# Kernel optimization log

Measured on AMD Instinct MI355X. Metric: run time of the kernel, lower is better.

## Reference

```python
import jax, jax.numpy as jnp
import numpy as np

DIM = 1024
HEADS = 16
DIM_HEAD = 64
INNER = HEADS * DIM_HEAD  # 1024
MLP = 4096
EPS = 1e-5


def setup_inputs() -> dict:
    key = jax.random.key(0)
    ks = jax.random.split(key, 8)
    s = lambda fan_in: 1.0 / np.sqrt(fan_in)
    return {
        "x": jax.random.normal(ks[0], (4, 2048, DIM), dtype=jnp.float32),
        "ln1_g": jnp.ones((DIM,), jnp.float32),
        "ln1_b": jnp.zeros((DIM,), jnp.float32),
        "w_qkv": jax.random.normal(ks[1], (DIM, 3 * INNER), jnp.float32) * s(DIM),
        "w_out": jax.random.normal(ks[2], (INNER, DIM), jnp.float32) * s(INNER),
        "b_out": jnp.zeros((DIM,), jnp.float32),
        "ln2_g": jnp.ones((DIM,), jnp.float32),
        "ln2_b": jnp.zeros((DIM,), jnp.float32),
        "w1": jax.random.normal(ks[3], (DIM, MLP), jnp.float32) * s(DIM),
        "b1": jnp.zeros((MLP,), jnp.float32),
        "w2": jax.random.normal(ks[4], (MLP, DIM), jnp.float32) * s(MLP),
        "b2": jnp.zeros((DIM,), jnp.float32),
    }


def _layernorm(x, g, b):
    mu = jnp.mean(x, axis=-1, keepdims=True)
    var = jnp.mean(jnp.square(x - mu), axis=-1, keepdims=True)
    return (x - mu) * jax.lax.rsqrt(var + EPS) * g + b


def _block(x, ln1_g, ln1_b, w_qkv, w_out, b_out, ln2_g, ln2_b, w1, b1, w2, b2):
    # pre-norm attention
    h = _layernorm(x, ln1_g, ln1_b)
    qkv = h @ w_qkv  # [b, n, 3*inner]
    q, k, v = jnp.split(qkv, 3, axis=-1)
    def heads(t):  # b n (h d) -> b h n d
        b, n, _ = t.shape
        return t.reshape(b, n, HEADS, DIM_HEAD).transpose(0, 2, 1, 3)
    q, k, v = heads(q), heads(k), heads(v)
    scale = DIM_HEAD ** -0.5
    dots = jnp.einsum("bhnd,bhmd->bhnm", q, k) * scale
    attn = jax.nn.softmax(dots, axis=-1)
    out = jnp.einsum("bhnm,bhmd->bhnd", attn, v)
    b, _, n, _ = out.shape
    out = out.transpose(0, 2, 1, 3).reshape(b, n, INNER)
    x = out @ w_out + b_out + x
    # pre-norm FFN
    h = _layernorm(x, ln2_g, ln2_b)
    h = jax.nn.gelu(h @ w1 + b1, approximate=False)
    return h @ w2 + b2 + x


def reference(x, ln1_g, ln1_b, w_qkv, w_out, b_out, ln2_g, ln2_b, w1, b1, w2, b2):
    return _block(x, ln1_g, ln1_b, w_qkv, w_out, b_out, ln2_g, ln2_b, w1, b1, w2, b2)
```

## Files before the change

### kernel.cpp

```cpp
#include <hip/hip_runtime.h>
#include <hip/hip_bf16.h>
#include <math.h>


typedef __bf16 bf16;
typedef __bf16 bf16x8 __attribute__((ext_vector_type(8)));
typedef __bf16 bf16x4 __attribute__((ext_vector_type(4)));
typedef __bf16 bf16x2 __attribute__((ext_vector_type(2)));
typedef float  f32x4  __attribute__((ext_vector_type(4)));
typedef unsigned int u32;
typedef u32 u32x4 __attribute__((ext_vector_type(4)));

#define MFMA_16x16x32(a, b, c) __builtin_amdgcn_mfma_f32_16x16x32_bf16((a), (b), (c), 0, 0, 0)

#define SWAP32(x, y) asm("v_permlane32_swap_b32 %0, %1" : "+v"(x), "+v"(y))
#define SWAP16(x, y) asm("v_permlane16_swap_b32 %0, %1" : "+v"(x), "+v"(y))

__device__ __forceinline__ void gl_lds16(const void* g, void* l) {
    __builtin_amdgcn_global_load_lds(
        (const __attribute__((address_space(1))) u32*)g,
        (__attribute__((address_space(3))) u32*)l, 16, 0, 0);
}

__device__ __forceinline__ u32 pack_bf16x2(float a, float b) {
    bf16x2 t; t[0] = (bf16)a; t[1] = (bf16)b;
    return __builtin_bit_cast(u32, t);
}

__device__ __forceinline__ float fast_gelu(float x) {
    const float u = x * (0.7978845608028654f + 0.03567740814183f * x * x);
    const float e = __builtin_amdgcn_exp2f(u * 2.8853900817779268f);
    return x * e * __builtin_amdgcn_rcpf(e + 1.0f);
}

__global__ __launch_bounds__(256) void transpose_f32_bf16(
    const float* __restrict__ in, bf16* __restrict__ out, int R, int C)
{
    __shared__ float tile[32][33];
    const int cb = blockIdx.x * 32, rb = blockIdx.y * 32;
    const int c = threadIdx.x & 31, r0 = threadIdx.x >> 5;
#pragma unroll
    for (int i = 0; i < 4; ++i) {
        int r = r0 + i * 8;
        tile[r][c] = in[(size_t)(rb + r) * C + cb + c];
    }
    __syncthreads();
#pragma unroll
    for (int i = 0; i < 4; ++i) {
        int rr = r0 + i * 8;
        out[(size_t)(cb + rr) * R + rb + c] = (bf16)tile[c][rr];
    }
}

__global__ __launch_bounds__(256) void transpose_v(
    const bf16* __restrict__ qkv, bf16* __restrict__ VT)
{
    __shared__ float tile[32][33];
    const int tokb = blockIdx.x * 32;
    const int db   = blockIdx.y * 32;
    const int bh   = blockIdx.z;
    const int b = bh >> 4, h = bh & 15;
    const int c = threadIdx.x & 31, r0 = threadIdx.x >> 5;
#pragma unroll
    for (int i = 0; i < 4; ++i) {
        int r = r0 + i * 8;
        tile[r][c] = (float)qkv[(size_t)(b * 2048 + tokb + r) * 3072 + 2048 + h * 64 + db + c];
    }
    __syncthreads();
#pragma unroll
    for (int i = 0; i < 4; ++i) {
        int rr = r0 + i * 8;
        VT[((size_t)bh * 64 + db + rr) * 2048 + tokb + c] = (bf16)tile[c][rr];
    }
}

__global__ __launch_bounds__(256) void ln_kernel(
    const float* __restrict__ x, const float* __restrict__ g,
    const float* __restrict__ b, bf16* __restrict__ out)
{
    const int lane = threadIdx.x & 63;
    const int wv   = threadIdx.x >> 6;
    const size_t token = (size_t)blockIdx.x * 4 + wv;
    const float* xr = x + token * 1024;
    float4 v[4];
    float s = 0.f, ss = 0.f;
#pragma unroll
    for (int c = 0; c < 4; ++c) {
        v[c] = *(const float4*)(xr + c * 256 + lane * 4);
        s  += v[c].x + v[c].y + v[c].z + v[c].w;
        ss += v[c].x * v[c].x + v[c].y * v[c].y + v[c].z * v[c].z + v[c].w * v[c].w;
    }
#pragma unroll
    for (int off = 32; off > 0; off >>= 1) {
        s  += __shfl_xor(s, off);
        ss += __shfl_xor(ss, off);
    }
    const float mu  = s * (1.0f / 1024.0f);
    const float var = ss * (1.0f / 1024.0f) - mu * mu;
    const float rs  = rsqrtf(var + 1e-5f);
    bf16* orow = out + token * 1024;
#pragma unroll
    for (int c = 0; c < 4; ++c) {
        float4 gg = *(const float4*)(g + c * 256 + lane * 4);
        float4 bb = *(const float4*)(b + c * 256 + lane * 4);
        bf16x4 o;
        o[0] = (bf16)((v[c].x - mu) * rs * gg.x + bb.x);
        o[1] = (bf16)((v[c].y - mu) * rs * gg.y + bb.y);
        o[2] = (bf16)((v[c].z - mu) * rs * gg.z + bb.z);
        o[3] = (bf16)((v[c].w - mu) * rs * gg.w + bb.w);
        *(bf16x4*)(orow + c * 256 + lane * 4) = o;
    }
}

template <int EPI>
__global__ __launch_bounds__(256, 4) void gemm_bt(
    const bf16* __restrict__ A, const bf16* __restrict__ Bt,
    const float* __restrict__ bias, const float* __restrict__ resid,
    void* __restrict__ outp, int M, int N, int K)
{
    __shared__ __align__(16) bf16 sA[128 * 64];
    __shared__ __align__(16) bf16 sB[128 * 64];

    const int tid  = threadIdx.x;
    const int lane = tid & 63;
    const int wv   = tid >> 6;
    const int quad = lane >> 4;
    const int l16  = lane & 15;

    const int id  = blockIdx.x;
    const int xcd = id & 7, j = id >> 3;
    const int M0 = (xcd * 8 + (j & 7)) * 128;
    const int N0 = (j >> 3) * 128;

    const int wm = (wv >> 1) * 64;
    const int wn = (wv & 1) * 64;

    f32x4 acc[4][4] = {};

    const bf16* paG[4];
    const bf16* pbG[4];
#pragma unroll
    for (int c = 0; c < 4; ++c) {
        const int f = c * 256 + tid;
        const int row = f >> 3;
        const int gch = (f & 7) ^ (row & 7);
        paG[c] = A  + (size_t)(M0 + row) * K + gch * 8;
        pbG[c] = Bt + (size_t)(N0 + row) * K + gch * 8;
    }

    const int sw = l16 & 7;

    for (int k0 = 0; k0 < K; k0 += 64) {
        __syncthreads();
#pragma unroll
        for (int c = 0; c < 4; ++c) {
            const int f8 = (c * 256 + tid) * 8;
            gl_lds16(paG[c] + k0, sA + f8);
            gl_lds16(pbG[c] + k0, sB + f8);
        }
        __syncthreads();

#pragma unroll
        for (int s = 0; s < 2; ++s) {
            const int chp = (s * 4 + quad) ^ sw;
            bf16x8 af[4], bfr[4];
#pragma unroll
            for (int t = 0; t < 4; ++t)
                af[t] = *(const bf16x8*)(sA + ((wm + t * 16 + l16) << 6) + chp * 8);
#pragma unroll
            for (int t = 0; t < 4; ++t)
                bfr[t] = *(const bf16x8*)(sB + ((wn + t * 16 + l16) << 6) + chp * 8);
#pragma unroll
            for (int tm = 0; tm < 4; ++tm)
#pragma unroll
                for (int tn = 0; tn < 4; ++tn)
                    acc[tm][tn] = MFMA_16x16x32(bfr[tn], af[tm], acc[tm][tn]);
        }
    }

#pragma unroll
    for (int tm = 0; tm < 4; ++tm) {
        const int row = M0 + wm + tm * 16 + l16;
#pragma unroll
        for (int tn = 0; tn < 4; ++tn) {
            const int col = N0 + wn + tn * 16 + quad * 4;
            const size_t idx = (size_t)row * N + col;
            const f32x4 v = acc[tm][tn];
            if (EPI == 0) {
                bf16x4 o;
#pragma unroll
                for (int r = 0; r < 4; ++r) o[r] = (bf16)v[r];
                *(bf16x4*)((bf16*)outp + idx) = o;
            } else if (EPI == 1) {
                const f32x4 b4 = *(const f32x4*)(bias + col);
                const f32x4 r4 = *(const f32x4*)(resid + idx);
                *(f32x4*)((float*)outp + idx) = v + b4 + r4;
            } else {
                const f32x4 b4 = *(const f32x4*)(bias + col);
                bf16x4 o;
#pragma unroll
                for (int r = 0; r < 4; ++r) o[r] = (bf16)fast_gelu(v[r] + b4[r]);
                *(bf16x4*)((bf16*)outp + idx) = o;
            }
        }
    }
}

#define BAR256()  asm volatile("s_barrier" ::: "memory")
#define WAITVM(n) asm volatile("s_waitcnt vmcnt(" #n ")" ::: "memory")
#define WAITLG()  do { asm volatile("s_waitcnt lgkmcnt(0)" ::: "memory"); \
                       __builtin_amdgcn_sched_barrier(0); } while (0)

template <int EPI>
__global__ __launch_bounds__(512, 2) void gemm256(
    const bf16* __restrict__ A, const bf16* __restrict__ Bt,
    const float* __restrict__ bias, void* __restrict__ outp,
    int N, int K)
{
    __shared__ __align__(16) bf16 sA[2][16384];
    __shared__ __align__(16) bf16 sB[2][16384];

    const int tid  = threadIdx.x;
    const int lane = tid & 63;
    const int wv   = tid >> 6;
    const int quad = lane >> 4;
    const int l16  = lane & 15;
    const int wr   = wv >> 2;
    const int wc   = wv & 3;

    const int id = blockIdx.x;
    const int wg = (id & 7) * ((int)gridDim.x >> 3) + (id >> 3);
    const int M0 = (wg & 31) * 256;
    const int N0 = (wg >> 5) * 256;

    const int srow = tid >> 3;
    const int sch  = (tid & 7) ^ (srow & 7);
    const bf16* gA = A  + (size_t)(M0 + srow) * K + sch * 8;
    const bf16* gB = Bt + (size_t)(N0 + srow) * K + sch * 8;
    const size_t r64  = (size_t)64 * K;
    const size_t r128 = (size_t)128 * K;

    f32x4 acc[8][4] = {};
    bf16x8 af[4][2], bf0[2][2], bf1[2][2];

    auto STG = [&](const bf16* g, bf16* l) {
        gl_lds16(g, l + tid * 8);
        gl_lds16(g + r64, l + tid * 8 + 4096);
    };
    auto LDA = [&](int buf, int mh) {
#pragma unroll
        for (int tm = 0; tm < 4; ++tm) {
            const int row = wr * 128 + mh * 64 + tm * 16 + l16;
            const bf16* p = &sA[buf][row * 64];
            const int swz = (row & 7) << 3;
            af[tm][0] = *(const bf16x8*)(p + (( quad      << 3) ^ swz));
            af[tm][1] = *(const bf16x8*)(p + (((quad + 4) << 3) ^ swz));
        }
    };
    auto LDB = [&](int buf, int nh, bf16x8 (&bfr)[2][2]) {
#pragma unroll
        for (int tn = 0; tn < 2; ++tn) {
            const int row = wc * 64 + nh * 32 + tn * 16 + l16;
            const bf16* p = &sB[buf][row * 64];
            const int swz = (row & 7) << 3;
            bfr[tn][0] = *(const bf16x8*)(p + (( quad      << 3) ^ swz));
            bfr[tn][1] = *(const bf16x8*)(p + (((quad + 4) << 3) ^ swz));
        }
    };
    auto MM = [&](int mh, int nh, bf16x8 (&bfr)[2][2]) {
        __builtin_amdgcn_s_setprio(1);
#pragma unroll
        for (int tm = 0; tm < 4; ++tm)
#pragma unroll
            for (int tn = 0; tn < 2; ++tn) {
                f32x4& a = acc[mh * 4 + tm][nh * 2 + tn];
                a = MFMA_16x16x32(bfr[tn][0], af[tm][0], a);
                a = MFMA_16x16x32(bfr[tn][1], af[tm][1], a);
            }
        __builtin_amdgcn_s_setprio(0);
    };

    STG(gA,              &sA[0][0]);
    STG(gA + r128,       &sA[0][8192]);
    STG(gB,              &sB[0][0]);
    STG(gB + r128,       &sB[0][8192]);
    STG(gB + 64,         &sB[1][0]);
    STG(gB + r128 + 64,  &sB[1][8192]);
    WAITVM(4);
    BAR256();

    const int NU = K >> 7;
#pragma unroll 1
    for (int u = 0; u < NU; ++u) {
        const size_t k1 = (size_t)(2 * u + 1) * 64;
        const size_t k2 = (size_t)(2 * u + 2) * 64;
        const size_t k3 = (size_t)(2 * u + 3) * 64;
        const bool more = (u + 1 < NU);

        LDA(0, 0); LDB(0, 0, bf0);
        STG(gA + k1, &sA[1][0]);
        BAR256(); WAITLG(); MM(0, 0, bf0); BAR256();

        LDB(0, 1, bf1);
        STG(gA + r128 + k1, &sA[1][8192]);
        BAR256(); WAITLG(); MM(0, 1, bf1); BAR256();

        LDA(0, 1);
        if (more) STG(gB + k2, &sB[0][0]);
        BAR256(); WAITLG(); MM(1, 1, bf1); BAR256();

        if (more) STG(gB + r128 + k2, &sB[0][8192]);
        BAR256(); MM(1, 0, bf0);
        if (more) { WAITVM(4); } else { WAITVM(0); }
        BAR256();

        LDA(1, 0); LDB(1, 0, bf0);
        if (more) STG(gA + k2, &sA[0][0]);
        BAR256(); WAITLG(); MM(0, 0, bf0); BAR256();

        LDB(1, 1, bf1);
        if (more) STG(gA + r128 + k2, &sA[0][8192]);
        BAR256(); WAITLG(); MM(0, 1, bf1); BAR256();

        LDA(1, 1);
        if (more) STG(gB + k3, &sB[1][0]);
        BAR256(); WAITLG(); MM(1, 1, bf1); BAR256();

        if (more) {
            STG(gB + r128 + k3, &sB[1][8192]);
            BAR256(); MM(1, 0, bf0);
            WAITVM(4);
            BAR256();
        } else {
            BAR256(); MM(1, 0, bf0);
        }
    }

#pragma unroll
    for (int tm = 0; tm < 8; ++tm) {
        const int row = M0 + wr * 128 + (tm >> 2) * 64 + (tm & 3) * 16 + l16;
#pragma unroll
        for (int tn = 0; tn < 4; ++tn) {
            const int col = N0 + wc * 64 + (tn >> 1) * 32 + (tn & 1) * 16 + quad * 4;
            const size_t idx = (size_t)row * N + col;
            const f32x4 v = acc[tm][tn];
            if (EPI == 0) {
                bf16x4 o;
#pragma unroll
                for (int r = 0; r < 4; ++r) o[r] = (bf16)v[r];
                *(bf16x4*)((bf16*)outp + idx) = o;
            } else {
                const f32x4 b4 = *(const f32x4*)(bias + col);
                bf16x4 o;
#pragma unroll
                for (int r = 0; r < 4; ++r) o[r] = (bf16)fast_gelu(v[r] + b4[r]);
                *(bf16x4*)((bf16*)outp + idx) = o;
            }
        }
    }
}

__global__ __launch_bounds__(256, 4) void attn_kernel(
    const bf16* __restrict__ qkv, const bf16* __restrict__ VT,
    bf16* __restrict__ attn_out)
{
    __shared__ __align__(16) bf16 sK[4096];
    __shared__ __align__(16) bf16 sV[4096];

    const int bh = blockIdx.y, b = bh >> 4, h = bh & 15;
    const int tid = threadIdx.x, lane = tid & 63, wv = tid >> 6;
    const int quad = lane >> 4, l16 = lane & 15;
    const size_t tok0 = (size_t)b * 2048;
    const int q0 = blockIdx.x * 128 + wv * 32;

    bf16x8 qf[2][2];
#pragma unroll
    for (int mi = 0; mi < 2; ++mi)
#pragma unroll
        for (int c = 0; c < 2; ++c) {
            bf16x8 t = *(const bf16x8*)(qkv + (tok0 + q0 + mi * 16 + l16) * 3072 + h * 64 + c * 32 + quad * 8);
#pragma unroll
            for (int j = 0; j < 8; ++j) t[j] = (bf16)((float)t[j] * 0.18033688011112042f);
            qf[mi][c] = t;
        }

    f32x4 o[2][4] = {};
    float lsum[2] = {0.f, 0.f};

    const int fA = tid, fB = tid + 256;
    const int cKA = fA >> 8, keyA = (fA >> 2) & 63, qcA = fA & 3;
    const int cKB = fB >> 8, keyB = (fB >> 2) & 63, qcB = fB & 3;
    const int dVA = fA >> 3, ccA = fA & 7;
    const int dVB = fB >> 3, ccB = fB & 7;
    const bf16* Kb = qkv + 1024 + h * 64;
    const bf16* Vb = VT + (size_t)bh * 64 * 2048;

    for (int kt = 0; kt < 32; ++kt) {
        const int kb = kt * 64;
        __syncthreads();
        gl_lds16(Kb + (tok0 + kb + keyA) * 3072 + cKA * 32 + ((qcA ^ (keyA & 3)) * 8), sK + fA * 8);
        gl_lds16(Kb + (tok0 + kb + keyB) * 3072 + cKB * 32 + ((qcB ^ (keyB & 3)) * 8), sK + fB * 8);
        gl_lds16(Vb + (size_t)dVA * 2048 + kb + ((ccA ^ (dVA & 7)) * 8), sV + fA * 8);
        gl_lds16(Vb + (size_t)dVB * 2048 + kb + ((ccB ^ (dVB & 7)) * 8), sV + fB * 8);
        __syncthreads();

        u32 w[2][4][2];
        __builtin_amdgcn_s_setprio(1);
#pragma unroll
        for (int ct = 0; ct < 4; ++ct) {
            const int key = ct * 16 + l16;
            const int ch = quad ^ (l16 & 3);
            bf16x8 k0 = *(const bf16x8*)(sK + (key * 4 + ch) * 8);
            bf16x8 k1 = *(const bf16x8*)(sK + (256 + key * 4 + ch) * 8);
#pragma unroll
            for (int mi = 0; mi < 2; ++mi) {
                f32x4 z = {};
                z = MFMA_16x16x32(k0, qf[mi][0], z);
                z = MFMA_16x16x32(k1, qf[mi][1], z);
                float p0 = __builtin_amdgcn_exp2f(z[0]);
                float p1 = __builtin_amdgcn_exp2f(z[1]);
                float p2 = __builtin_amdgcn_exp2f(z[2]);
                float p3 = __builtin_amdgcn_exp2f(z[3]);
                lsum[mi] += (p0 + p1) + (p2 + p3);
                w[mi][ct][0] = pack_bf16x2(p0, p1);
                w[mi][ct][1] = pack_bf16x2(p2, p3);
            }
        }
        __builtin_amdgcn_s_setprio(0);

        bf16x8 pa[2][2];
#pragma unroll
        for (int mi = 0; mi < 2; ++mi) {
            u32 pw0[4], pw1[4];
#pragma unroll
            for (int c2 = 0; c2 < 2; ++c2) {
                u32 x = w[mi][0][c2], y = w[mi][1][c2];
                SWAP32(x, y); SWAP16(x, y);
                pw0[c2] = x; pw0[2 + c2] = y;
                u32 x2 = w[mi][2][c2], y2 = w[mi][3][c2];
                SWAP32(x2, y2); SWAP16(x2, y2);
                pw1[c2] = x2; pw1[2 + c2] = y2;
            }
            u32x4 t0 = {pw0[0], pw0[1], pw0[2], pw0[3]};
            u32x4 t1 = {pw1[0], pw1[1], pw1[2], pw1[3]};
            pa[mi][0] = __builtin_bit_cast(bf16x8, t0);
            pa[mi][1] = __builtin_bit_cast(bf16x8, t1);
        }

        __builtin_amdgcn_s_setprio(1);
#pragma unroll
        for (int dt = 0; dt < 4; ++dt) {
            const int d = dt * 16 + l16;
            bf16x8 v0 = *(const bf16x8*)(sV + (d * 8 + (quad ^ (l16 & 7))) * 8);
            bf16x8 v1 = *(const bf16x8*)(sV + (d * 8 + ((quad + 4) ^ (l16 & 7))) * 8);
#pragma unroll
            for (int mi = 0; mi < 2; ++mi) {
                o[mi][dt] = MFMA_16x16x32(pa[mi][0], v0, o[mi][dt]);
                o[mi][dt] = MFMA_16x16x32(pa[mi][1], v1, o[mi][dt]);
            }
        }
        __builtin_amdgcn_s_setprio(0);
    }

#pragma unroll
    for (int mi = 0; mi < 2; ++mi) {
        float t = lsum[mi];
        t += __shfl_xor(t, 16);
        t += __shfl_xor(t, 32);
        float rl[4];
#pragma unroll
        for (int r = 0; r < 4; ++r) rl[r] = 1.0f / __shfl(t, quad * 4 + r);
#pragma unroll
        for (int dt = 0; dt < 4; ++dt)
#pragma unroll
            for (int r = 0; r < 4; ++r) {
                const size_t tok = tok0 + q0 + mi * 16 + quad * 4 + r;
                attn_out[tok * 1024 + h * 64 + dt * 16 + l16] = (bf16)(o[mi][dt][r] * rl[r]);
            }
    }
}

extern "C" void kernel_launch(void* const* d_in, const int* in_sizes, int n_in,
                              void* d_out, int out_size, void* d_ws, size_t ws_size,
                              hipStream_t stream)
{
    const float* x     = (const float*)d_in[0];
    const float* ln1_g = (const float*)d_in[1];
    const float* ln1_b = (const float*)d_in[2];
    const float* w_qkv = (const float*)d_in[3];
    const float* w_out = (const float*)d_in[4];
    const float* b_out = (const float*)d_in[5];
    const float* ln2_g = (const float*)d_in[6];
    const float* ln2_b = (const float*)d_in[7];
    const float* w1    = (const float*)d_in[8];
    const float* b1    = (const float*)d_in[9];
    const float* w2    = (const float*)d_in[10];
    const float* b2    = (const float*)d_in[11];
    float* out = (float*)d_out;

    char* ws = (char*)d_ws;
    bf16*  h      = (bf16*)(ws);
    bf16*  big    = (bf16*)(ws + 16777216);
    bf16*  attn_o = (bf16*)(ws + 83886080);
    float* x_mid  = (float*)(ws + 100663296);
    bf16*  VT     = (bf16*)(ws + 100663296);
    bf16*  wT_qkv = (bf16*)(ws + 134217728);
    bf16*  wT_out = (bf16*)(ws + 140509184);
    bf16*  wT_1   = (bf16*)(ws + 142606336);
    bf16*  wT_2   = (bf16*)(ws + 150994944);

    transpose_f32_bf16<<<dim3(3072/32, 1024/32), 256, 0, stream>>>(w_qkv, wT_qkv, 1024, 3072);
    transpose_f32_bf16<<<dim3(1024/32, 1024/32), 256, 0, stream>>>(w_out, wT_out, 1024, 1024);
    transpose_f32_bf16<<<dim3(4096/32, 1024/32), 256, 0, stream>>>(w1,    wT_1,   1024, 4096);
    transpose_f32_bf16<<<dim3(1024/32, 4096/32), 256, 0, stream>>>(w2,    wT_2,   4096, 1024);

    ln_kernel<<<2048, 256, 0, stream>>>(x, ln1_g, ln1_b, h);

    gemm_bt<0><<<64 * 24, 256, 0, stream>>>(h, wT_qkv, nullptr, nullptr, big, 8192, 3072, 1024);

    transpose_v<<<dim3(64, 2, 64), 256, 0, stream>>>(big, VT);

    attn_kernel<<<dim3(16, 64), 256, 0, stream>>>(big, VT, attn_o);

    gemm_bt<1><<<64 * 8, 256, 0, stream>>>(attn_o, wT_out, b_out, x, x_mid, 8192, 1024, 1024);

    ln_kernel<<<2048, 256, 0, stream>>>(x_mid, ln2_g, ln2_b, h);

    gemm256<2><<<512, 512, 0, stream>>>(h, wT_1, b1, big, 4096, 1024);

    gemm_bt<1><<<64 * 8, 256, 0, stream>>>(big, wT_2, b2, x_mid, out, 8192, 1024, 4096);
}
```

Before: 505.8 us.

## Fuse weight transposes with first layernorm and rebalance FFN GEMM tile choices

The four weight-transpose launches and the first layernorm are merged into a single prep kernel that dispatches on block index, removing several launches. The W1 GEMM moves from the 256x256 kernel to the generic 128-tile gemm_bt with the GELU epilogue. The W2 GEMM (K=4096) now uses a new 256x128-tile variant of the 256-thread-pair kernel with a residual epilogue, so larger tiles serve the long-K reduction. This trades tile shapes between the two FFN GEMMs. With N=1024 the W2 grid is only 256 blocks, which risks underfilling the device.

```diff
diff --git a/kernel.cpp b/kernel.cpp
--- a/kernel.cpp
+++ b/kernel.cpp
@@ -33,11 +33,11 @@
     return x * e * __builtin_amdgcn_rcpf(e + 1.0f);
 }
 
-__global__ __launch_bounds__(256) void transpose_f32_bf16(
-    const float* __restrict__ in, bf16* __restrict__ out, int R, int C)
-{
-    __shared__ float tile[32][33];
-    const int cb = blockIdx.x * 32, rb = blockIdx.y * 32;
+__device__ __forceinline__ void transpose_body(
+    const float* __restrict__ in, bf16* __restrict__ out, int R, int C,
+    int bx, int by, float (*tile)[33])
+{
+    const int cb = bx * 32, rb = by * 32;
     const int c = threadIdx.x & 31, r0 = threadIdx.x >> 5;
 #pragma unroll
     for (int i = 0; i < 4; ++i) {
@@ -52,35 +52,13 @@
     }
 }
 
-__global__ __launch_bounds__(256) void transpose_v(
-    const bf16* __restrict__ qkv, bf16* __restrict__ VT)
-{
-    __shared__ float tile[32][33];
-    const int tokb = blockIdx.x * 32;
-    const int db   = blockIdx.y * 32;
-    const int bh   = blockIdx.z;
-    const int b = bh >> 4, h = bh & 15;
-    const int c = threadIdx.x & 31, r0 = threadIdx.x >> 5;
-#pragma unroll
-    for (int i = 0; i < 4; ++i) {
-        int r = r0 + i * 8;
-        tile[r][c] = (float)qkv[(size_t)(b * 2048 + tokb + r) * 3072 + 2048 + h * 64 + db + c];
-    }
-    __syncthreads();
-#pragma unroll
-    for (int i = 0; i < 4; ++i) {
-        int rr = r0 + i * 8;
-        VT[((size_t)bh * 64 + db + rr) * 2048 + tokb + c] = (bf16)tile[c][rr];
-    }
-}
-
-__global__ __launch_bounds__(256) void ln_kernel(
+__device__ __forceinline__ void ln_body(
     const float* __restrict__ x, const float* __restrict__ g,
-    const float* __restrict__ b, bf16* __restrict__ out)
+    const float* __restrict__ b, bf16* __restrict__ out, int bid)
 {
     const int lane = threadIdx.x & 63;
     const int wv   = threadIdx.x >> 6;
-    const size_t token = (size_t)blockIdx.x * 4 + wv;
+    const size_t token = (size_t)bid * 4 + wv;
     const float* xr = x + token * 1024;
     float4 v[4];
     float s = 0.f, ss = 0.f;
@@ -112,6 +90,61 @@
     }
 }
 
+__global__ __launch_bounds__(256) void prep_kernel(
+    const float* __restrict__ w_qkv, const float* __restrict__ w_out,
+    const float* __restrict__ w1,    const float* __restrict__ w2,
+    bf16* __restrict__ wT_qkv, bf16* __restrict__ wT_out,
+    bf16* __restrict__ wT_1,   bf16* __restrict__ wT_2,
+    const float* __restrict__ x, const float* __restrict__ g,
+    const float* __restrict__ b, bf16* __restrict__ h)
+{
+    __shared__ float tile[32][33];
+    const int id = blockIdx.x;
+    if (id < 3072) {
+        transpose_body(w_qkv, wT_qkv, 1024, 3072, id % 96, id / 96, tile);
+    } else if (id < 4096) {
+        const int j = id - 3072;
+        transpose_body(w_out, wT_out, 1024, 1024, j & 31, j >> 5, tile);
+    } else if (id < 8192) {
+        const int j = id - 4096;
+        transpose_body(w1, wT_1, 1024, 4096, j & 127, j >> 7, tile);
+    } else if (id < 12288) {
+        const int j = id - 8192;
+        transpose_body(w2, wT_2, 4096, 1024, j & 31, j >> 5, tile);
+    } else {
+        ln_body(x, g, b, h, id - 12288);
+    }
+}
+
+__global__ __launch_bounds__(256) void ln_kernel(
+    const float* __restrict__ x, const float* __restrict__ g,
+    const float* __restrict__ b, bf16* __restrict__ out)
+{
+    ln_body(x, g, b, out, blockIdx.x);
+}
+
+__global__ __launch_bounds__(256) void transpose_v(
+    const bf16* __restrict__ qkv, bf16* __restrict__ VT)
+{
+    __shared__ float tile[32][33];
+    const int tokb = blockIdx.x * 32;
+    const int db   = blockIdx.y * 32;
+    const int bh   = blockIdx.z;
+    const int b = bh >> 4, h = bh & 15;
+    const int c = threadIdx.x & 31, r0 = threadIdx.x >> 5;
+#pragma unroll
+    for (int i = 0; i < 4; ++i) {
+        int r = r0 + i * 8;
+        tile[r][c] = (float)qkv[(size_t)(b * 2048 + tokb + r) * 3072 + 2048 + h * 64 + db + c];
+    }
+    __syncthreads();
+#pragma unroll
+    for (int i = 0; i < 4; ++i) {
+        int rr = r0 + i * 8;
+        VT[((size_t)bh * 64 + db + rr) * 2048 + tokb + c] = (bf16)tile[c][rr];
+    }
+}
+
 template <int EPI>
 __global__ __launch_bounds__(256, 4) void gemm_bt(
     const bf16* __restrict__ A, const bf16* __restrict__ Bt,
@@ -212,13 +245,13 @@
                        __builtin_amdgcn_sched_barrier(0); } while (0)
 
 template <int EPI>
-__global__ __launch_bounds__(512, 2) void gemm256(
+__global__ __launch_bounds__(512, 2) void gemm256n(
     const bf16* __restrict__ A, const bf16* __restrict__ Bt,
-    const float* __restrict__ bias, void* __restrict__ outp,
-    int N, int K)
+    const float* __restrict__ bias, const float* __restrict__ resid,
+    void* __restrict__ outp, int N, int K)
 {
     __shared__ __align__(16) bf16 sA[2][16384];
-    __shared__ __align__(16) bf16 sB[2][16384];
+    __shared__ __align__(16) bf16 sB[2][8192];
 
     const int tid  = threadIdx.x;
     const int lane = tid & 63;
@@ -230,8 +263,8 @@
 
     const int id = blockIdx.x;
     const int wg = (id & 7) * ((int)gridDim.x >> 3) + (id >> 3);
-    const int M0 = (wg & 31) * 256;
-    const int N0 = (wg >> 5) * 256;
+    const int M0 = (wg >> 3) * 256;
+    const int N0 = (wg & 7) * 128;
 
     const int srow = tid >> 3;
     const int sch  = (tid & 7) ^ (srow & 7);
@@ -240,8 +273,8 @@
     const size_t r64  = (size_t)64 * K;
     const size_t r128 = (size_t)128 * K;
 
-    f32x4 acc[8][4] = {};
-    bf16x8 af[4][2], bf0[2][2], bf1[2][2];
+    f32x4 acc[8][2] = {};
+    bf16x8 af[4][2], bf0[2], bf1[2];
 
     auto STG = [&](const bf16* g, bf16* l) {
         gl_lds16(g, l + tid * 8);
@@ -257,36 +290,29 @@
             af[tm][1] = *(const bf16x8*)(p + (((quad + 4) << 3) ^ swz));
         }
     };
-    auto LDB = [&](int buf, int nh, bf16x8 (&bfr)[2][2]) {
-#pragma unroll
-        for (int tn = 0; tn < 2; ++tn) {
-            const int row = wc * 64 + nh * 32 + tn * 16 + l16;
-            const bf16* p = &sB[buf][row * 64];
-            const int swz = (row & 7) << 3;
-            bfr[tn][0] = *(const bf16x8*)(p + (( quad      << 3) ^ swz));
-            bfr[tn][1] = *(const bf16x8*)(p + (((quad + 4) << 3) ^ swz));
-        }
+    auto LDB = [&](int buf, int nh, bf16x8 (&bfr)[2]) {
+        const int row = wc * 32 + nh * 16 + l16;
+        const bf16* p = &sB[buf][row * 64];
+        const int swz = (row & 7) << 3;
+        bfr[0] = *(const bf16x8*)(p + (( quad      << 3) ^ swz));
+        bfr[1] = *(const bf16x8*)(p + (((quad + 4) << 3) ^ swz));
     };
-    auto MM = [&](int mh, int nh, bf16x8 (&bfr)[2][2]) {
+    auto MM = [&](int mh, int nh, bf16x8 (&bfr)[2]) {
         __builtin_amdgcn_s_setprio(1);
 #pragma unroll
-        for (int tm = 0; tm < 4; ++tm)
-#pragma unroll
-            for (int tn = 0; tn < 2; ++tn) {
-                f32x4& a = acc[mh * 4 + tm][nh * 2 + tn];
-                a = MFMA_16x16x32(bfr[tn][0], af[tm][0], a);
-                a = MFMA_16x16x32(bfr[tn][1], af[tm][1], a);
-            }
+        for (int tm = 0; tm < 4; ++tm) {
+            f32x4& a = acc[mh * 4 + tm][nh];
+            a = MFMA_16x16x32(bfr[0], af[tm][0], a);
+            a = MFMA_16x16x32(bfr[1], af[tm][1], a);
+        }
         __builtin_amdgcn_s_setprio(0);
     };
 
-    STG(gA,              &sA[0][0]);
-    STG(gA + r128,       &sA[0][8192]);
-    STG(gB,              &sB[0][0]);
-    STG(gB + r128,       &sB[0][8192]);
-    STG(gB + 64,         &sB[1][0]);
-    STG(gB + r128 + 64,  &sB[1][8192]);
-    WAITVM(4);
+    STG(gA,         &sA[0][0]);
+    STG(gA + r128,  &sA[0][8192]);
+    STG(gB,         &sB[0][0]);
+    STG(gB + 64,    &sB[1][0]);
+    WAITVM(2);
     BAR256();
 
     const int NU = K >> 7;
@@ -309,9 +335,8 @@
         if (more) STG(gB + k2, &sB[0][0]);
         BAR256(); WAITLG(); MM(1, 1, bf1); BAR256();
 
-        if (more) STG(gB + r128 + k2, &sB[0][8192]);
         BAR256(); MM(1, 0, bf0);
-        if (more) { WAITVM(4); } else { WAITVM(0); }
+        if (more) { WAITVM(2); } else { WAITVM(0); }
         BAR256();
 
         LDA(1, 0); LDB(1, 0, bf0);
@@ -327,9 +352,8 @@
         BAR256(); WAITLG(); MM(1, 1, bf1); BAR256();
 
         if (more) {
-            STG(gB + r128 + k3, &sB[1][8192]);
             BAR256(); MM(1, 0, bf0);
-            WAITVM(4);
+            WAITVM(2);
             BAR256();
         } else {
             BAR256(); MM(1, 0, bf0);
@@ -337,18 +361,22 @@
     }
 
 #pragma unroll
-    for (int tm = 0; tm < 8; ++tm) {
-        const int row = M0 + wr * 128 + (tm >> 2) * 64 + (tm & 3) * 16 + l16;
-#pragma unroll
-        for (int tn = 0; tn < 4; ++tn) {
-            const int col = N0 + wc * 64 + (tn >> 1) * 32 + (tn & 1) * 16 + quad * 4;
+    for (int a8 = 0; a8 < 8; ++a8) {
+        const int row = M0 + wr * 128 + (a8 >> 2) * 64 + (a8 & 3) * 16 + l16;
+#pragma unroll
+        for (int tn = 0; tn < 2; ++tn) {
+            const int col = N0 + wc * 32 + tn * 16 + quad * 4;
             const size_t idx = (size_t)row * N + col;
-            const f32x4 v = acc[tm][tn];
+            const f32x4 v = acc[a8][tn];
             if (EPI == 0) {
                 bf16x4 o;
 #pragma unroll
                 for (int r = 0; r < 4; ++r) o[r] = (bf16)v[r];
                 *(bf16x4*)((bf16*)outp + idx) = o;
+            } else if (EPI == 1) {
+                const f32x4 b4 = *(const f32x4*)(bias + col);
+                const f32x4 r4 = *(const f32x4*)(resid + idx);
+                *(f32x4*)((float*)outp + idx) = v + b4 + r4;
             } else {
                 const f32x4 b4 = *(const f32x4*)(bias + col);
                 bf16x4 o;
@@ -509,12 +537,9 @@
     bf16*  wT_1   = (bf16*)(ws + 142606336);
     bf16*  wT_2   = (bf16*)(ws + 150994944);
 
-    transpose_f32_bf16<<<dim3(3072/32, 1024/32), 256, 0, stream>>>(w_qkv, wT_qkv, 1024, 3072);
-    transpose_f32_bf16<<<dim3(1024/32, 1024/32), 256, 0, stream>>>(w_out, wT_out, 1024, 1024);
-    transpose_f32_bf16<<<dim3(4096/32, 1024/32), 256, 0, stream>>>(w1,    wT_1,   1024, 4096);
-    transpose_f32_bf16<<<dim3(1024/32, 4096/32), 256, 0, stream>>>(w2,    wT_2,   4096, 1024);
-
-    ln_kernel<<<2048, 256, 0, stream>>>(x, ln1_g, ln1_b, h);
+    prep_kernel<<<14336, 256, 0, stream>>>(w_qkv, w_out, w1, w2,
+                                           wT_qkv, wT_out, wT_1, wT_2,
+                                           x, ln1_g, ln1_b, h);
 
     gemm_bt<0><<<64 * 24, 256, 0, stream>>>(h, wT_qkv, nullptr, nullptr, big, 8192, 3072, 1024);
 
@@ -526,7 +551,7 @@
 
     ln_kernel<<<2048, 256, 0, stream>>>(x_mid, ln2_g, ln2_b, h);
 
-    gemm256<2><<<512, 512, 0, stream>>>(h, wT_1, b1, big, 4096, 1024);
-
-    gemm_bt<1><<<64 * 8, 256, 0, stream>>>(big, wT_2, b2, x_mid, out, 8192, 1024, 4096);
-}
+    gemm_bt<2><<<64 * 32, 256, 0, stream>>>(h, wT_1, b1, nullptr, big, 8192, 4096, 1024);
+
+    gemm256n<1><<<256, 512, 0, stream>>>(big, wT_2, b2, x_mid, out, 1024, 4096);
+}
```

New measurement: 460.3 us. 1.1x faster.
